# Kernel tuning notes

Hardware: AMD Instinct MI355X
Metric: run time of the kernel (lower is better)

## Reference

```python
import jax, jax.numpy as jnp
import numpy as np

KH = KW = 3
STRIDE = 1
PAD = 1
DIL = 1


def _conv2d(x, w, b):
    out = jax.lax.conv_general_dilated(
        x, w, (STRIDE, STRIDE), [(PAD, PAD), (PAD, PAD)],
        rhs_dilation=(DIL, DIL), dimension_numbers=('NCHW', 'OIHW', 'NCHW'))
    return out + b[None, :, None, None]


def _bilinear_sample(x, ys, xs):
    # x: [B,C,H,W]; ys, xs: [B,K,Ho,Wo] float sampling coords (zero padding outside)
    B, C, H, W = x.shape
    y0 = jnp.floor(ys)
    x0 = jnp.floor(xs)
    wy1 = ys - y0
    wx1 = xs - x0
    wy0 = 1.0 - wy1
    wx0 = 1.0 - wx1
    x_flat = x.reshape(B, C, H * W)

    def gather(yc, xc):
        valid = (yc >= 0) & (yc <= H - 1) & (xc >= 0) & (xc <= W - 1)
        yi = jnp.clip(yc, 0, H - 1).astype(jnp.int32)
        xi = jnp.clip(xc, 0, W - 1).astype(jnp.int32)
        idx = yi * W + xi  # [B,K,Ho,Wo]
        g = jax.vmap(lambda xb, ib: xb[:, ib.reshape(-1)])(x_flat, idx)
        g = g.reshape(B, C, *idx.shape[1:])  # [B,C,K,Ho,Wo]
        return g * valid[:, None].astype(x.dtype)

    return (gather(y0, x0) * (wy0 * wx0)[:, None]
            + gather(y0, x0 + 1) * (wy0 * wx1)[:, None]
            + gather(y0 + 1, x0) * (wy1 * wx0)[:, None]
            + gather(y0 + 1, x0 + 1) * (wy1 * wx1)[:, None])


def setup_inputs() -> dict:
    key = jax.random.key(0)
    ks = jax.random.split(key, 6)
    B, C, H, W = 8, 256, 64, 64
    Cout = 256
    K = KH * KW
    x = jax.random.normal(ks[0], (B, C, H, W), jnp.float32)
    # small random offset/mask heads (module inits them to zero; random keeps the
    # irregular-gather path exercised with modest, realistic offsets)
    w_offset = jax.random.normal(ks[1], (2 * K, C, KH, KW), jnp.float32) * 0.01
    b_offset = jax.random.normal(ks[2], (2 * K,), jnp.float32) * 0.1
    w_mask = jax.random.normal(ks[3], (K, C, KH, KW), jnp.float32) * 0.01
    b_mask = jnp.zeros((K,), jnp.float32)
    stdv = 1.0 / np.sqrt(C * KH * KW)
    weight = jax.random.uniform(ks[4], (Cout, C, KH, KW), jnp.float32, -stdv, stdv)
    bias = jnp.zeros((Cout,), jnp.float32)
    return {"x": x, "w_offset": w_offset, "b_offset": b_offset,
            "w_mask": w_mask, "b_mask": b_mask, "weight": weight, "bias": bias}


def reference(x, w_offset, b_offset, w_mask, b_mask, weight, bias):
    B, C, H, W = x.shape
    K = KH * KW
    offset = _conv2d(x, w_offset, b_offset)          # [B, 2K, Ho, Wo]
    mask = jax.nn.sigmoid(_conv2d(x, w_mask, b_mask))  # [B, K, Ho, Wo]
    Ho, Wo = offset.shape[2], offset.shape[3]
    off = offset.reshape(B, K, 2, Ho, Wo)
    dy, dx = off[:, :, 0], off[:, :, 1]              # (dy, dx) pairs per kernel tap
    ky = jnp.arange(KH, dtype=x.dtype) * DIL - PAD
    kx = jnp.arange(KW, dtype=x.dtype) * DIL - PAD
    kyf = jnp.repeat(ky, KW)   # [K]
    kxf = jnp.tile(kx, KH)     # [K]
    ys = jnp.arange(Ho, dtype=x.dtype)[None, None, :, None] * STRIDE + kyf[None, :, None, None] + dy
    xs = jnp.arange(Wo, dtype=x.dtype)[None, None, None, :] * STRIDE + kxf[None, :, None, None] + dx
    sampled = _bilinear_sample(x, ys, xs) * mask[:, None]  # [B,C,K,Ho,Wo]
    out = jnp.einsum('bckhw,ock->bohw', sampled, weight.reshape(weight.shape[0], C, K))
    return out + bias[None, :, None, None]
```

## Files before the change

### kernel.cpp

```cpp
#include <hip/hip_runtime.h>
#include <math.h>


typedef __bf16 bf16x8 __attribute__((ext_vector_type(8)));
typedef float  f32x4  __attribute__((ext_vector_type(4)));
typedef float  f32x2  __attribute__((ext_vector_type(2)));
typedef int    i32x4  __attribute__((ext_vector_type(4)));
typedef unsigned short u16x8 __attribute__((ext_vector_type(8)));
typedef unsigned short u16x4 __attribute__((ext_vector_type(4)));

__device__ __forceinline__ unsigned short f2b(float f) {
  return __builtin_bit_cast(unsigned short, (__bf16)f);
}
__device__ __forceinline__ float blo(unsigned u) {
  return __builtin_bit_cast(float, u << 16);
}
__device__ __forceinline__ float bhi(unsigned u) {
  return __builtin_bit_cast(float, u & 0xffff0000u);
}

__global__ __launch_bounds__(256) void prep(const float* __restrict__ x,
                                            unsigned short* __restrict__ xt,
                                            const float* __restrict__ w,
                                            const float* __restrict__ wo,
                                            const float* __restrict__ wm,
                                            __bf16* __restrict__ wp,
                                            __bf16* __restrict__ womp) {
  __shared__ float tile[64][65];
  const int t = threadIdx.x;
  if (blockIdx.x < 2048) {
    const int bid = blockIdx.x;
    const int b = bid & 7, rem = bid >> 3;
    const int cc = rem & 3, hw0 = (rem >> 2) << 6;
    const int a = t & 63, g = t >> 6;
#pragma unroll
    for (int r = 0; r < 16; ++r) {
      int crow = (r << 2) + g;
      tile[crow][a] = x[(((b << 8) + (cc << 6) + crow) << 12) + hw0 + a];
    }
    __syncthreads();
    const int a0 = (t & 15) << 2, gg = t >> 4;
#pragma unroll
    for (int r = 0; r < 4; ++r) {
      int hwr = (r << 4) + gg;
      u16x4 v;
#pragma unroll
      for (int j = 0; j < 4; ++j) v[j] = f2b(tile[a0 + j][hwr]);
      *(u16x4*)&xt[((b << 12) + hw0 + hwr) * 256 + (cc << 6) + a0] = v;
    }
  } else if (blockIdx.x < 4352) {
    int idx = (blockIdx.x - 2048) * 256 + t;
    int o = idx / 2304, rem = idx - o * 2304;
    int c = rem / 9, k = rem - c * 9;
    wp[(((k << 5) + (c >> 3)) * 256 + o) * 8 + (c & 7)] = (__bf16)w[idx];
  } else {
    int idx = (blockIdx.x - 4352) * 256 + t;
    if (idx >= 32 * 256 * 9) return;
    int r = idx / 2304, rem = idx - r * 2304;
    int c = rem / 9, k = rem - c * 9;
    float v = 0.f;
    if (r < 18) v = wo[((r << 8) + c) * 9 + k];
    else if (r < 27) v = wm[(((r - 18) << 8) + c) * 9 + k];
    womp[(((k << 5) + (c >> 3)) * 32 + r) * 8 + (c & 7)] = (__bf16)v;
  }
}

__global__ __launch_bounds__(512, 2) void deform_fused(
    const unsigned short* __restrict__ xt, const __bf16* __restrict__ wp,
    const __bf16* __restrict__ womp, const float* __restrict__ b_off,
    const float* __restrict__ b_msk, const float* __restrict__ bias,
    float* __restrict__ out) {
  const int bi = blockIdx.x & 7, h = blockIdx.x >> 3;
  const int t = threadIdx.x, lane = t & 63, wv = t >> 6;
  const int l16 = lane & 15, lh = lane >> 4;
  __shared__ __align__(16) unsigned short S[4][64 * 64];
  __shared__ __align__(16) float samp[9][64][8];
  __shared__ __align__(16) float offm[27][64];

  const int sp = t >> 3;
  const int sc0 = (t & 7) << 3;
  const int wofs = (sp << 6) + ((((t & 7) ^ (sp & 7)) & 7) << 3);
  const unsigned short* xtb = xt + ((long)bi << 20);

  {
    f32x4 oacc0 = {}, oacc1 = {};
    const int mf = wv & 1, nf = wv >> 1;

    auto PLOAD = [&](int it, u16x8& r) {
      const int k = it >> 2, cc = it & 3;
      const int hh = h + k / 3 - 1;
      const int ww = sp + (k % 3) - 1;
      const bool valid = (hh >= 0) & (hh < 64) & (ww >= 0) & (ww < 64);
      r = valid ? *(const u16x8*)(xtb + (((hh << 6) + ww) << 8) + (cc << 6) + sc0)
                : u16x8{};
    };
    auto PMFMA = [&](int it, int buf) {
      const int k = it >> 2, cc = it & 3;
#pragma unroll
      for (int kk = 0; kk < 2; ++kk) {
        const int prow = (nf << 4) + l16;
        const int gi = (kk << 2) | lh;
        bf16x8 bfrag = *(const bf16x8*)&S[buf][(prow << 6) + (((gi ^ (prow & 7)) & 7) << 3)];
        const __bf16* ap =
            womp + ((((k << 5) + (cc << 3) + (kk << 2) + lh) << 5) + (mf << 4) + l16) * 8;
        bf16x8 af = *(const bf16x8*)ap;
        if (kk == 0)
          oacc0 = __builtin_amdgcn_mfma_f32_16x16x32_bf16(af, bfrag, oacc0, 0, 0, 0);
        else
          oacc1 = __builtin_amdgcn_mfma_f32_16x16x32_bf16(af, bfrag, oacc1, 0, 0, 0);
      }
    };

    u16x8 p0, p1;
    PLOAD(0, p0);
    PLOAD(1, p1);
    *(u16x8*)&S[0][wofs] = p0;
    *(u16x8*)&S[1][wofs] = p1;
    __syncthreads();
    for (int p = 0; p < 18; ++p) {
      const int base = (p & 1) << 1;
      const int nb = base ^ 2;
      if (p < 17) {
        PLOAD((p << 1) + 2, p0);
        PLOAD((p << 1) + 3, p1);
      }
      PMFMA(p << 1, base);
      PMFMA((p << 1) + 1, base | 1);
      if (p < 17) {
        *(u16x8*)&S[nb][wofs] = p0;
        *(u16x8*)&S[nb | 1][wofs] = p1;
      }
      __syncthreads();
    }

    f32x4 oacc = oacc0 + oacc1;
    const int px = (nf << 4) + l16;
#pragma unroll
    for (int r = 0; r < 4; ++r) {
      int row = (mf << 4) + (lh << 2) + r;
      if (row < 18) {
        offm[row][px] = oacc[r] + b_off[row];
      } else if (row < 27) {
        float v = oacc[r] + b_msk[row - 18];
        offm[row][px] = 1.f / (1.f + expf(-v));
      }
    }
    __syncthreads();
  }

  for (int i = t; i < 576; i += 512) {
    int k = i >> 6, p = i & 63;
    float dy = offm[(k << 1)][p], dx = offm[(k << 1) + 1][p], mk = offm[18 + k][p];
    float ys = (float)(h + k / 3 - 1) + dy;
    float xs = (float)(p + k % 3 - 1) + dx;
    float y0f = floorf(ys), x0f = floorf(xs);
    int iy0 = (int)y0f, ix0 = (int)x0f;
    float wy1 = ys - y0f, wx1 = xs - x0f;
    float wy0 = 1.f - wy1, wx0 = 1.f - wx1;
    float w00 = wy0 * wx0 * mk, w01 = wy0 * wx1 * mk;
    float w10 = wy1 * wx0 * mk, w11 = wy1 * wx1 * mk;
    if (iy0 < 0 || iy0 > 63) { w00 = 0.f; w01 = 0.f; }
    if (iy0 < -1 || iy0 > 62) { w10 = 0.f; w11 = 0.f; }
    if (ix0 < 0 || ix0 > 63) { w00 = 0.f; w10 = 0.f; }
    if (ix0 < -1 || ix0 > 62) { w01 = 0.f; w11 = 0.f; }
    const int cy0 = min(max(iy0, 0), 63), cy1 = min(max(iy0 + 1, 0), 63);
    const int cx0 = min(max(ix0, 0), 63), cx1 = min(max(ix0 + 1, 0), 63);
    samp[k][p][0] = w00; samp[k][p][1] = w01;
    samp[k][p][2] = w10; samp[k][p][3] = w11;
    samp[k][p][4] = __builtin_bit_cast(float, (((cy0 << 6) + cx0) << 8));
    samp[k][p][5] = __builtin_bit_cast(float, (((cy0 << 6) + cx1) << 8));
    samp[k][p][6] = __builtin_bit_cast(float, (((cy1 << 6) + cx0) << 8));
    samp[k][p][7] = __builtin_bit_cast(float, (((cy1 << 6) + cx1) << 8));
  }
  __syncthreads();

  f32x4 acc[2][4] = {};

  auto GATHER = [&](int it, u16x8* r, f32x4& w4) {
    const int k = it >> 2, cc = it & 3;
    w4 = *(const f32x4*)&samp[k][sp][0];
    i32x4 o4 = __builtin_bit_cast(i32x4, *(const f32x4*)&samp[k][sp][4]);
    const int c0 = (cc << 6) + sc0;
    r[0] = *(const u16x8*)(xtb + o4.x + c0);
    r[1] = *(const u16x8*)(xtb + o4.y + c0);
    r[2] = *(const u16x8*)(xtb + o4.z + c0);
    r[3] = *(const u16x8*)(xtb + o4.w + c0);
  };

  auto STEP = [&](int it, const u16x8* r, const f32x4& w4, int buf) {
    u16x8 sv;
    const unsigned* u0 = (const unsigned*)&r[0];
    const unsigned* u1 = (const unsigned*)&r[1];
    const unsigned* u2 = (const unsigned*)&r[2];
    const unsigned* u3 = (const unsigned*)&r[3];
#pragma unroll
    for (int j = 0; j < 4; ++j) {
      f32x2 a{blo(u0[j]), bhi(u0[j])};
      f32x2 b{blo(u1[j]), bhi(u1[j])};
      f32x2 c{blo(u2[j]), bhi(u2[j])};
      f32x2 d{blo(u3[j]), bhi(u3[j])};
      f32x2 s = a * w4.x;
      s += b * w4.y;
      s += c * w4.z;
      s += d * w4.w;
      sv[2 * j]     = f2b(s.x);
      sv[2 * j + 1] = f2b(s.y);
    }
    *(u16x8*)&S[buf][wofs] = sv;
    __syncthreads();
    const int k = it >> 2, cc = it & 3;
#pragma unroll
    for (int kk = 0; kk < 2; ++kk) {
      bf16x8 bfr[4];
#pragma unroll
      for (int nf = 0; nf < 4; ++nf) {
        const int prow = (nf << 4) + l16;
        const int gi = (kk << 2) | lh;
        bfr[nf] = *(const bf16x8*)&S[buf][(prow << 6) + (((gi ^ (prow & 7)) & 7) << 3)];
      }
#pragma unroll
      for (int mf = 0; mf < 2; ++mf) {
        const int orow = (wv << 5) + (mf << 4) + l16;
        const __bf16* ap = wp + ((((k << 5) + (cc << 3) + (kk << 2) + lh) << 8) + orow) * 8;
        bf16x8 af = *(const bf16x8*)ap;
#pragma unroll
        for (int nf = 0; nf < 4; ++nf)
          acc[mf][nf] = __builtin_amdgcn_mfma_f32_16x16x32_bf16(af, bfr[nf], acc[mf][nf], 0, 0, 0);
      }
    }
  };

  u16x8 rA[4], rB[4];
  f32x4 wA, wB;
  GATHER(0, rA, wA);
  for (int it = 0; it < 36; it += 2) {
    GATHER(it + 1, rB, wB);
    STEP(it, rA, wA, 0);
    if (it + 2 < 36) GATHER(it + 2, rA, wA);
    STEP(it + 1, rB, wB, 1);
  }

#pragma unroll
  for (int mf = 0; mf < 2; ++mf) {
    const int o = (wv << 5) + (mf << 4) + (lh << 2);
    f32x4 bv = *(const f32x4*)(bias + o);
#pragma unroll
    for (int nf = 0; nf < 4; ++nf) {
      const int p = (nf << 4) + l16;
      const int hw = (h << 6) + p;
#pragma unroll
      for (int r = 0; r < 4; ++r)
        out[(((bi << 8) + o + r) << 12) + hw] = acc[mf][nf][r] + bv[r];
    }
  }
}

extern "C" void kernel_launch(void* const* d_in, const int* in_sizes, int n_in,
                              void* d_out, int out_size, void* d_ws, size_t ws_size,
                              hipStream_t stream) {
  (void)in_sizes; (void)n_in; (void)out_size; (void)ws_size;
  const float* x        = (const float*)d_in[0];
  const float* w_offset = (const float*)d_in[1];
  const float* b_offset = (const float*)d_in[2];
  const float* w_mask   = (const float*)d_in[3];
  const float* b_mask   = (const float*)d_in[4];
  const float* weight   = (const float*)d_in[5];
  const float* bias     = (const float*)d_in[6];
  float* out = (float*)d_out;

  char* ws = (char*)d_ws;
  unsigned short* xt = (unsigned short*)(ws);
  __bf16* Wpack  = (__bf16*)(ws + 16777216);
  __bf16* Womp   = (__bf16*)(ws + 17956864);

  prep<<<4640, 256, 0, stream>>>(x, xt, weight, w_offset, w_mask, Wpack, Womp);
  deform_fused<<<512, 512, 0, stream>>>(xt, Wpack, Womp, b_offset, b_mask, bias, out);
}
```

Baseline: 86.05 us.

## Split each output row across two blocks and split offset-conv K across waves

Each block now handles half an image row (32 pixels) instead of 64, doubling the grid to 1024 blocks so more blocks are resident across the CUs. Per-thread gathers shrink to 4 channels. The offset/mask conv work is split across two wave groups by tap-chunk parity, with partial sums reduced through shared scratch. The cost is that each block reloads the full weight tiles for only half the pixels, doubling weight traffic per output, and MFMA work per sync is smaller.

```diff
diff --git a/kernel.cpp b/kernel.cpp
--- a/kernel.cpp
+++ b/kernel.cpp
@@ -70,32 +70,36 @@
     const __bf16* __restrict__ womp, const float* __restrict__ b_off,
     const float* __restrict__ b_msk, const float* __restrict__ bias,
     float* __restrict__ out) {
-  const int bi = blockIdx.x & 7, h = blockIdx.x >> 3;
+  const int bi = blockIdx.x & 7, remb = blockIdx.x >> 3;
+  const int h = remb >> 1, halfb = remb & 1;
+  const int pxbase = (h << 6) + (halfb << 5);
   const int t = threadIdx.x, lane = t & 63, wv = t >> 6;
   const int l16 = lane & 15, lh = lane >> 4;
-  __shared__ __align__(16) unsigned short S[4][64 * 64];
-  __shared__ __align__(16) float samp[9][64][8];
-  __shared__ __align__(16) float offm[27][64];
-
-  const int sp = t >> 3;
-  const int sc0 = (t & 7) << 3;
-  const int wofs = (sp << 6) + ((((t & 7) ^ (sp & 7)) & 7) << 3);
+  __shared__ __align__(16) unsigned short S[4][32 * 64];
+  __shared__ __align__(16) float samp[9][32][8];
+  __shared__ __align__(16) float offm[27][32];
+
+  const int sp = t >> 4;
+  const int tc = t & 15;
+  const int sc0 = tc << 2;
+  const int wofs = (sp << 6) + ((((tc >> 1) ^ (sp & 7)) & 7) << 3) + ((tc & 1) << 2);
   const unsigned short* xtb = xt + ((long)bi << 20);
+  float* pscr = (float*)samp;
 
   {
-    f32x4 oacc0 = {}, oacc1 = {};
-    const int mf = wv & 1, nf = wv >> 1;
-
-    auto PLOAD = [&](int it, u16x8& r) {
+    f32x4 oacc = {};
+    const int mf = wv & 1, nf = (wv >> 1) & 1, khalf = wv >> 2;
+
+    auto PLOAD = [&](int it, u16x4& r) {
       const int k = it >> 2, cc = it & 3;
       const int hh = h + k / 3 - 1;
-      const int ww = sp + (k % 3) - 1;
+      const int ww = (halfb << 5) + sp + (k % 3) - 1;
       const bool valid = (hh >= 0) & (hh < 64) & (ww >= 0) & (ww < 64);
-      r = valid ? *(const u16x8*)(xtb + (((hh << 6) + ww) << 8) + (cc << 6) + sc0)
-                : u16x8{};
+      r = valid ? *(const u16x4*)(xtb + (((hh << 6) + ww) << 8) + (cc << 6) + sc0)
+                : u16x4{};
     };
-    auto PMFMA = [&](int it, int buf) {
-      const int k = it >> 2, cc = it & 3;
+    auto PMFMA = [&](int c, int buf) {
+      const int k = c >> 2, cc = c & 3;
 #pragma unroll
       for (int kk = 0; kk < 2; ++kk) {
         const int prow = (nf << 4) + l16;
@@ -104,18 +108,15 @@
         const __bf16* ap =
             womp + ((((k << 5) + (cc << 3) + (kk << 2) + lh) << 5) + (mf << 4) + l16) * 8;
         bf16x8 af = *(const bf16x8*)ap;
-        if (kk == 0)
-          oacc0 = __builtin_amdgcn_mfma_f32_16x16x32_bf16(af, bfrag, oacc0, 0, 0, 0);
-        else
-          oacc1 = __builtin_amdgcn_mfma_f32_16x16x32_bf16(af, bfrag, oacc1, 0, 0, 0);
+        oacc = __builtin_amdgcn_mfma_f32_16x16x32_bf16(af, bfrag, oacc, 0, 0, 0);
       }
     };
 
-    u16x8 p0, p1;
+    u16x4 p0, p1;
     PLOAD(0, p0);
     PLOAD(1, p1);
-    *(u16x8*)&S[0][wofs] = p0;
-    *(u16x8*)&S[1][wofs] = p1;
+    *(u16x4*)&S[0][wofs] = p0;
+    *(u16x4*)&S[1][wofs] = p1;
     __syncthreads();
     for (int p = 0; p < 18; ++p) {
       const int base = (p & 1) << 1;
@@ -124,35 +125,40 @@
         PLOAD((p << 1) + 2, p0);
         PLOAD((p << 1) + 3, p1);
       }
-      PMFMA(p << 1, base);
-      PMFMA((p << 1) + 1, base | 1);
+      PMFMA((p << 1) | khalf, base | khalf);
       if (p < 17) {
-        *(u16x8*)&S[nb][wofs] = p0;
-        *(u16x8*)&S[nb | 1][wofs] = p1;
+        *(u16x4*)&S[nb][wofs] = p0;
+        *(u16x4*)&S[nb | 1][wofs] = p1;
       }
       __syncthreads();
     }
 
-    f32x4 oacc = oacc0 + oacc1;
-    const int px = (nf << 4) + l16;
-#pragma unroll
-    for (int r = 0; r < 4; ++r) {
-      int row = (mf << 4) + (lh << 2) + r;
-      if (row < 18) {
-        offm[row][px] = oacc[r] + b_off[row];
-      } else if (row < 27) {
-        float v = oacc[r] + b_msk[row - 18];
-        offm[row][px] = 1.f / (1.f + expf(-v));
-      }
-    }
-    __syncthreads();
-  }
-
-  for (int i = t; i < 576; i += 512) {
-    int k = i >> 6, p = i & 63;
+    if (khalf == 1) *(f32x4*)&pscr[(((mf << 1) | nf) << 8) + (lane << 2)] = oacc;
+    __syncthreads();
+    if (khalf == 0) {
+      f32x4 o2 = *(const f32x4*)&pscr[(((mf << 1) | nf) << 8) + (lane << 2)];
+      oacc += o2;
+      const int px = (nf << 4) + l16;
+#pragma unroll
+      for (int r = 0; r < 4; ++r) {
+        int row = (mf << 4) + (lh << 2) + r;
+        if (row < 18) {
+          offm[row][px] = oacc[r] + b_off[row];
+        } else if (row < 27) {
+          float v = oacc[r] + b_msk[row - 18];
+          offm[row][px] = 1.f / (1.f + expf(-v));
+        }
+      }
+    }
+    __syncthreads();
+  }
+
+  for (int i = t; i < 288; i += 512) {
+    int k = i >> 5, p = i & 31;
+    int pw = (halfb << 5) + p;
     float dy = offm[(k << 1)][p], dx = offm[(k << 1) + 1][p], mk = offm[18 + k][p];
     float ys = (float)(h + k / 3 - 1) + dy;
-    float xs = (float)(p + k % 3 - 1) + dx;
+    float xs = (float)(pw + k % 3 - 1) + dx;
     float y0f = floorf(ys), x0f = floorf(xs);
     int iy0 = (int)y0f, ix0 = (int)x0f;
     float wy1 = ys - y0f, wx1 = xs - x0f;
@@ -174,27 +180,27 @@
   }
   __syncthreads();
 
-  f32x4 acc[2][4] = {};
-
-  auto GATHER = [&](int it, u16x8* r, f32x4& w4) {
+  f32x4 acc[2][2] = {};
+
+  auto GATHER = [&](int it, u16x4* r, f32x4& w4) {
     const int k = it >> 2, cc = it & 3;
     w4 = *(const f32x4*)&samp[k][sp][0];
     i32x4 o4 = __builtin_bit_cast(i32x4, *(const f32x4*)&samp[k][sp][4]);
     const int c0 = (cc << 6) + sc0;
-    r[0] = *(const u16x8*)(xtb + o4.x + c0);
-    r[1] = *(const u16x8*)(xtb + o4.y + c0);
-    r[2] = *(const u16x8*)(xtb + o4.z + c0);
-    r[3] = *(const u16x8*)(xtb + o4.w + c0);
+    r[0] = *(const u16x4*)(xtb + o4.x + c0);
+    r[1] = *(const u16x4*)(xtb + o4.y + c0);
+    r[2] = *(const u16x4*)(xtb + o4.z + c0);
+    r[3] = *(const u16x4*)(xtb + o4.w + c0);
   };
 
-  auto STEP = [&](int it, const u16x8* r, const f32x4& w4, int buf) {
-    u16x8 sv;
+  auto STEP = [&](int it, const u16x4* r, const f32x4& w4, int buf) {
+    u16x4 sv;
     const unsigned* u0 = (const unsigned*)&r[0];
     const unsigned* u1 = (const unsigned*)&r[1];
     const unsigned* u2 = (const unsigned*)&r[2];
     const unsigned* u3 = (const unsigned*)&r[3];
 #pragma unroll
-    for (int j = 0; j < 4; ++j) {
+    for (int j = 0; j < 2; ++j) {
       f32x2 a{blo(u0[j]), bhi(u0[j])};
       f32x2 b{blo(u1[j]), bhi(u1[j])};
       f32x2 c{blo(u2[j]), bhi(u2[j])};
@@ -206,14 +212,14 @@
       sv[2 * j]     = f2b(s.x);
       sv[2 * j + 1] = f2b(s.y);
     }
-    *(u16x8*)&S[buf][wofs] = sv;
+    *(u16x4*)&S[buf][wofs] = sv;
     __syncthreads();
     const int k = it >> 2, cc = it & 3;
 #pragma unroll
     for (int kk = 0; kk < 2; ++kk) {
-      bf16x8 bfr[4];
-#pragma unroll
-      for (int nf = 0; nf < 4; ++nf) {
+      bf16x8 bfr[2];
+#pragma unroll
+      for (int nf = 0; nf < 2; ++nf) {
         const int prow = (nf << 4) + l16;
         const int gi = (kk << 2) | lh;
         bfr[nf] = *(const bf16x8*)&S[buf][(prow << 6) + (((gi ^ (prow & 7)) & 7) << 3)];
@@ -224,13 +230,13 @@
         const __bf16* ap = wp + ((((k << 5) + (cc << 3) + (kk << 2) + lh) << 8) + orow) * 8;
         bf16x8 af = *(const bf16x8*)ap;
 #pragma unroll
-        for (int nf = 0; nf < 4; ++nf)
+        for (int nf = 0; nf < 2; ++nf)
           acc[mf][nf] = __builtin_amdgcn_mfma_f32_16x16x32_bf16(af, bfr[nf], acc[mf][nf], 0, 0, 0);
       }
     }
   };
 
-  u16x8 rA[4], rB[4];
+  u16x4 rA[4], rB[4];
   f32x4 wA, wB;
   GATHER(0, rA, wA);
   for (int it = 0; it < 36; it += 2) {
@@ -245,9 +251,9 @@
     const int o = (wv << 5) + (mf << 4) + (lh << 2);
     f32x4 bv = *(const f32x4*)(bias + o);
 #pragma unroll
-    for (int nf = 0; nf < 4; ++nf) {
+    for (int nf = 0; nf < 2; ++nf) {
       const int p = (nf << 4) + l16;
-      const int hw = (h << 6) + p;
+      const int hw = pxbase + p;
 #pragma unroll
       for (int r = 0; r < 4; ++r)
         out[(((bi << 8) + o + r) << 12) + hw] = acc[mf][nf][r] + bv[r];
@@ -274,5 +280,5 @@
   __bf16* Womp   = (__bf16*)(ws + 17956864);
 
   prep<<<4640, 256, 0, stream>>>(x, xt, weight, w_offset, w_mask, Wpack, Womp);
-  deform_fused<<<512, 512, 0, stream>>>(xt, Wpack, Womp, b_offset, b_mask, bias, out);
-}
+  deform_fused<<<1024, 512, 0, stream>>>(xt, Wpack, Womp, b_offset, b_mask, bias, out);
+}
```

Result: slower. 120.3 us (+39.8%).
